# Kernel optimization log

Measured on AMD Instinct MI355X. Metric: run time of the kernel, lower is better.

Reference implementation:

```python
import jax, jax.numpy as jnp
import numpy as np

D = 128          # embedding_size
K = 1024         # num_embedding
DECAY = 0.99
EPS = 1e-5
VQ_COMMIT = 0.25
B, T = 16, 4096


def setup_inputs() -> dict:
    key = jax.random.key(0)
    k1, k2, k3 = jax.random.split(key, 3)
    emb = jax.random.normal(k2, (D, K), dtype=jnp.float32)
    return {
        "input": jax.random.normal(k1, (B, T, D), dtype=jnp.float32),
        "embedding": emb,
        "cluster_size": jnp.zeros((K,), dtype=jnp.float32),
        "embedding_mean": emb.copy(),
    }


def reference(input, embedding, cluster_size, embedding_mean):
    # ---- quantize: squared-distance argmin over codebook ----
    flatten = input.reshape(-1, D)                                   # [N, D]
    dist = ((flatten ** 2).sum(1, keepdims=True)
            - 2.0 * flatten @ embedding
            + (embedding ** 2).sum(0, keepdims=True))                # [N, K]
    embedding_ind = jnp.argmin(dist, axis=1)                         # [N]
    code = embedding_ind.reshape(input.shape[:-1])                   # [B, T]

    # ---- dequantize: codebook gather ----
    quantize = jnp.take(embedding.T, code, axis=0)                   # [B, T, D]

    # ---- EMA codebook update (training mode) ----
    N = flatten.shape[0]
    counts = jax.ops.segment_sum(jnp.ones((N,), input.dtype), embedding_ind,
                                 num_segments=K)                     # [K]
    emb_sum = jax.ops.segment_sum(flatten, embedding_ind,
                                  num_segments=K).T                  # [D, K]
    new_cluster_size = cluster_size * DECAY + (1.0 - DECAY) * counts
    new_embedding_mean = embedding_mean * DECAY + (1.0 - DECAY) * emb_sum
    n = new_cluster_size.sum()
    cs = (new_cluster_size + EPS) / (n + K * EPS) * n
    new_embedding = new_embedding_mean / cs[None, :]                 # [D, K]

    # ---- straight-through estimator + commitment loss ----
    quantize_st = input + jax.lax.stop_gradient(quantize - input)
    diff = VQ_COMMIT * jnp.mean(
        (jax.lax.stop_gradient(quantize_st) - input) ** 2)

    return (quantize_st, diff, code,
            new_embedding, new_cluster_size, new_embedding_mean)
```

## Files before the change

kernel.cpp:

```cpp
#include <hip/hip_runtime.h>
#include <hip/hip_fp16.h>
#include <math.h>

#define D_ 128
#define K_ 1024
#define N_ 65536
#define DECAY_ 0.99f
#define OMD_ 0.01f
#define EPS_ 1e-5f
#define VQC_ 0.25f
#define M1_ 0.14f
#define M2_ 0.14f
#define BIAS_ 96.0f
#define CLMIN_ 0.5f
#define CLMAX_ 508.0f
#define WSEG 32

typedef __attribute__((ext_vector_type(8))) _Float16 half8;
typedef __attribute__((ext_vector_type(4))) float f32x4;

#define WOFF_CODE  0
#define WOFF_E2    65536
#define WOFF_CNT   66560
#define WOFF_SSQ   67584
#define WOFF_RCNT  67585
#define WOFF_BASE  67648
#define WOFF_CURS  68736
#define WOFF_ORDER 69760
#define WOFF_ET    136320
#define WOFF_PART  267392
#define WOFF_CSORT 398464
#define WOFF_RLIST 791680
#define WOFF_EF    857216

#define OOFF_Q     0
#define OOFF_DIFF  8388608
#define OOFF_CODE  8388609
#define OOFF_NEMB  8454145
#define OOFF_NCS   8585217
#define OOFF_NMEAN 8586241

__device__ __forceinline__ unsigned umin32(unsigned a, unsigned b) { return a < b ? a : b; }
__device__ __forceinline__ unsigned umax32(unsigned a, unsigned b) { return a > b ? a : b; }

__device__ __forceinline__ void gld16(const unsigned short* g, unsigned short* l) {
    __builtin_amdgcn_global_load_lds(
        (const __attribute__((address_space(1))) unsigned int*)g,
        (__attribute__((address_space(3))) unsigned int*)l, 16, 0, 0);
}

__launch_bounds__(256)
__global__ void k_prep(const float* __restrict__ E, float* __restrict__ Et,
                       unsigned short* __restrict__ Ef, float* __restrict__ e2,
                       int* __restrict__ cnt, float* __restrict__ part1) {
    __shared__ float tile[128 * 17];
    __shared__ float e2s[16];
    int tid = threadIdx.x;
    int b = blockIdx.x;
    int c0 = b * 16;
    if (b == 0) {
        for (int i = tid; i < 1026; i += 256) cnt[i] = 0;
    }
    #pragma unroll
    for (int i = 0; i < 8; ++i) part1[b * 2048 + i * 256 + tid] = 0.f;
    if (tid < 16) e2s[tid] = 0.f;
    #pragma unroll
    for (int i = 0; i < 8; ++i) {
        int idx = i * 256 + tid;
        int d = idx >> 4, cc = idx & 15;
        tile[d * 17 + cc] = E[d * K_ + c0 + cc];
    }
    __syncthreads();
    #pragma unroll
    for (int i = 0; i < 8; ++i) {
        int idx = i * 256 + tid;
        int cc = idx >> 7, d = idx & 127;
        Et[(size_t)(c0 + cc) * D_ + d] = tile[d * 17 + cc];
    }
    int L = tid & 63, s = tid >> 6;
    int cc = L & 15;
    int d0 = s * 32 + ((L >> 4) << 3);
    unsigned short h[8];
    float sq = 0.f;
    #pragma unroll
    for (int j = 0; j < 8; ++j) {
        float e = tile[(d0 + j) * 17 + cc];
        sq = fmaf(e, e, sq);
        h[j] = __half_as_ushort(__float2half(-2.f * e));
    }
    int T = b * 256 + tid;
    #pragma unroll
    for (int j = 0; j < 8; ++j) Ef[T * 8 + j] = h[j];
    atomicAdd(&e2s[cc], sq);
    __syncthreads();
    if (tid < 16) {
        e2[c0 + tid] = e2s[tid];
    }
}

__launch_bounds__(512, 2)
__global__ void k_argmin_mfma(const float* __restrict__ x, const unsigned short* __restrict__ Ef,
                              const float* __restrict__ e2,
                              int* __restrict__ code_i, float* __restrict__ code_f,
                              int* __restrict__ cnt, int* __restrict__ rcnt,
                              int* __restrict__ rlist, const float* __restrict__ Et) {
    __shared__ unsigned short Bs[3][8192];
    __shared__ float e2s[K_];
    int tid = threadIdx.x;
    int w = tid >> 6, L = tid & 63, quad = L >> 4, col = L & 15;
    int mg = w >> 1, ng = w & 1;
    int n0 = blockIdx.x * 128;

    for (int i = tid; i < K_; i += 512) e2s[i] = e2[i];

    half8 ah[2][4];
    #pragma unroll
    for (int mt = 0; mt < 2; ++mt) {
        int tok = n0 + (2 * mg + mt) * 16 + col;
        #pragma unroll
        for (int s = 0; s < 4; ++s) {
            const float* p = x + (size_t)tok * D_ + s * 32 + quad * 8;
            float4 u0 = *(const float4*)(p);
            float4 u1 = *(const float4*)(p + 4);
            ah[mt][s][0] = (_Float16)u0.x; ah[mt][s][1] = (_Float16)u0.y;
            ah[mt][s][2] = (_Float16)u0.z; ah[mt][s][3] = (_Float16)u0.w;
            ah[mt][s][4] = (_Float16)u1.x; ah[mt][s][5] = (_Float16)u1.y;
            ah[mt][s][6] = (_Float16)u1.z; ah[mt][s][7] = (_Float16)u1.w;
        }
    }

    unsigned k1[2][4], k2[2][4], k3[2][4];
    #pragma unroll
    for (int mt = 0; mt < 2; ++mt)
        #pragma unroll
        for (int r = 0; r < 4; ++r) {
            k1[mt][r] = 0xFFFFFFFFu; k2[mt][r] = 0xFFFFFFFFu; k3[mt][r] = 0xFFFFFFFFu;
        }

    __syncthreads();

    #pragma unroll
    for (int i = 0; i < 2; ++i) {
        int o = (w * 2 + i) * 512;
        gld16(Ef + o + L * 8, &Bs[0][o]);
    }
    #pragma unroll
    for (int i = 0; i < 2; ++i) {
        int o = (w * 2 + i) * 512;
        gld16(Ef + 8192 + o + L * 8, &Bs[1][o]);
    }

    #pragma unroll
    for (int q = 0; q < 16; ++q) {
        if (q < 15) asm volatile("s_waitcnt vmcnt(2)" ::: "memory");
        else        asm volatile("s_waitcnt vmcnt(0)" ::: "memory");
        __builtin_amdgcn_s_barrier();
        asm volatile("" ::: "memory");

        const unsigned short* Bp = &Bs[q % 3][0];

        float evb[2];
        #pragma unroll
        for (int nn = 0; nn < 2; ++nn)
            evb[nn] = e2s[q * 64 + (2 * ng + nn) * 16 + col] + BIAS_;
        f32x4 acc[2][2];
        #pragma unroll
        for (int mt = 0; mt < 2; ++mt)
            #pragma unroll
            for (int nn = 0; nn < 2; ++nn)
                #pragma unroll
                for (int r = 0; r < 4; ++r)
                    acc[mt][nn][r] = evb[nn];

        #pragma unroll
        for (int s = 0; s < 4; ++s) {
            half8 bh[2];
            #pragma unroll
            for (int nn = 0; nn < 2; ++nn) {
                int off = (((2 * ng + nn) * 4 + s) * 64 + L) * 8;
                bh[nn] = *(const half8*)(Bp + off);
            }
            #pragma unroll
            for (int nn = 0; nn < 2; ++nn)
                #pragma unroll
                for (int mt = 0; mt < 2; ++mt)
                    acc[mt][nn] = __builtin_amdgcn_mfma_f32_16x16x32_f16(ah[mt][s], bh[nn], acc[mt][nn], 0, 0, 0);
        }

        #pragma unroll
        for (int nn = 0; nn < 2; ++nn) {
            unsigned cb = (unsigned)(q * 64 + (2 * ng + nn) * 16 + col);
            #pragma unroll
            for (int mt = 0; mt < 2; ++mt)
                #pragma unroll
                for (int r = 0; r < 4; ++r) {
                    float dc = fminf(fmaxf(acc[mt][nn][r], CLMIN_), CLMAX_);
                    unsigned key = (__float_as_uint(dc) & 0xFFFFFC00u) | cb;
                    unsigned m1 = umax32(k1[mt][r], key);
                    k1[mt][r]   = umin32(k1[mt][r], key);
                    unsigned m2 = umax32(k2[mt][r], m1);
                    k2[mt][r]   = umin32(k2[mt][r], m1);
                    k3[mt][r]   = umin32(k3[mt][r], m2);
                }
        }

        if (q < 14) {
            const unsigned short* src = Ef + (q + 2) * 8192;
            int sl = (q + 2) % 3;
            #pragma unroll
            for (int i = 0; i < 2; ++i) {
                int o = (w * 2 + i) * 512;
                gld16(src + o + L * 8, &Bs[sl][o]);
            }
        }
    }

    __syncthreads();
    unsigned* mk1 = (unsigned*)&Bs[0][0];
    unsigned* mk2 = mk1 + 256;
    unsigned* mk3 = mk2 + 256;

    #pragma unroll
    for (int mt = 0; mt < 2; ++mt) {
        #pragma unroll
        for (int r = 0; r < 4; ++r) {
            unsigned a = k1[mt][r], b = k2[mt][r], c = k3[mt][r];
            #pragma unroll
            for (int m = 1; m < 16; m <<= 1) {
                unsigned ao = (unsigned)__shfl_xor((int)a, m);
                unsigned bo = (unsigned)__shfl_xor((int)b, m);
                unsigned co = (unsigned)__shfl_xor((int)c, m);
                unsigned t1 = umax32(a, ao);
                a           = umin32(a, ao);
                unsigned s2 = umin32(b, bo);
                unsigned u  = umax32(t1, s2);
                b           = umin32(t1, s2);
                c           = umin32(u, umin32(c, co));
            }
            if (col == 0) {
                int tl = (2 * mg + mt) * 16 + quad * 4 + r;
                mk1[tl * 2 + ng] = a;
                mk2[tl * 2 + ng] = b;
                mk3[tl * 2 + ng] = c;
            }
        }
    }
    __syncthreads();
    if (tid < 128) {
        unsigned a1 = mk1[tid * 2], b1 = mk1[tid * 2 + 1];
        unsigned a2 = mk2[tid * 2], b2 = mk2[tid * 2 + 1];
        unsigned a3 = mk3[tid * 2], b3 = mk3[tid * 2 + 1];
        unsigned t1 = umax32(a1, b1);
        unsigned kk1 = umin32(a1, b1);
        unsigned s2 = umin32(a2, b2);
        unsigned kk2 = umin32(t1, s2);
        unsigned u  = umax32(t1, s2);
        unsigned kk3 = umin32(u, umin32(a3, b3));

        int i1 = (int)(kk1 & 1023u), i2 = (int)(kk2 & 1023u);
        float d1 = __uint_as_float(kk1 & 0xFFFFFC00u);
        float d2 = __uint_as_float(kk2 & 0xFFFFFC00u);
        float d3 = __uint_as_float(kk3 & 0xFFFFFC00u);
        int tok = n0 + tid;

        if (d3 - d1 < M2_) {
            code_i[tok] = i1;
            code_f[tok] = (float)i1;
            atomicAdd(cnt + i1, 1);
            int p = atomicAdd(rcnt, 1);
            rlist[p] = tok;
        } else {
            int win = i1;
            if (d2 - d1 < M1_) {
                const float* xr = x  + (size_t)tok * D_;
                const float* ea = Et + (size_t)i1 * D_;
                const float* eb = Et + (size_t)i2 * D_;
                float s1 = 0.f, sB = 0.f;
                #pragma unroll 4
                for (int dd = 0; dd < D_; dd += 4) {
                    float4 xv = *(const float4*)(xr + dd);
                    float4 av = *(const float4*)(ea + dd);
                    float4 bv = *(const float4*)(eb + dd);
                    s1 = fmaf(xv.x, av.x, s1); s1 = fmaf(xv.y, av.y, s1);
                    s1 = fmaf(xv.z, av.z, s1); s1 = fmaf(xv.w, av.w, s1);
                    sB = fmaf(xv.x, bv.x, sB); sB = fmaf(xv.y, bv.y, sB);
                    sB = fmaf(xv.z, bv.z, sB); sB = fmaf(xv.w, bv.w, sB);
                }
                float ex1 = e2s[i1] - 2.f * s1;
                float ex2 = e2s[i2] - 2.f * sB;
                if (ex2 < ex1 || (ex2 == ex1 && i2 < i1)) win = i2;
            }
            code_i[tok] = win;
            code_f[tok] = (float)win;
            atomicAdd(cnt + win, 1);
        }
    }
}

__launch_bounds__(256)
__global__ void k_fix(const float* __restrict__ x, const float* __restrict__ Et,
                      const float* __restrict__ e2, const int* __restrict__ rcnt,
                      const int* __restrict__ rlist, int* __restrict__ code_i,
                      float* __restrict__ code_f, int* __restrict__ cnt) {
    __shared__ float4 xs[32];
    __shared__ float sd[8];
    __shared__ int   si[8];
    int tid = threadIdx.x;
    int lane = tid & 63, w = tid >> 6;
    int half = lane >> 5;
    int q32  = lane & 31;
    int slot = w * 2 + half;
    int nr = *rcnt;
    for (int it = blockIdx.x; it < nr; it += gridDim.x) {
        __syncthreads();
        int tok = rlist[it];
        if (tid < 32) xs[tid] = ((const float4*)(x + (size_t)tok * D_))[tid];
        __syncthreads();
        float4 xv = xs[q32];
        float bd = INFINITY; int bb = 0;
        for (int c0 = 0; c0 < K_; c0 += 8) {
            int c = c0 + slot;
            float4 e = ((const float4*)(Et + (size_t)c * D_))[q32];
            float dot = xv.x * e.x + xv.y * e.y + xv.z * e.z + xv.w * e.w;
            dot += __shfl_xor(dot, 1);
            dot += __shfl_xor(dot, 2);
            dot += __shfl_xor(dot, 4);
            dot += __shfl_xor(dot, 8);
            dot += __shfl_xor(dot, 16);
            float dist = e2[c] - 2.f * dot;
            if (dist < bd) { bd = dist; bb = c; }
        }
        if (q32 == 0) { sd[slot] = bd; si[slot] = bb; }
        __syncthreads();
        if (tid == 0) {
            float fb = sd[0]; int fi = si[0];
            #pragma unroll
            for (int s = 1; s < 8; ++s) {
                if (sd[s] < fb || (sd[s] == fb && si[s] < fi)) { fb = sd[s]; fi = si[s]; }
            }
            int ob = code_i[tok];
            if (fi != ob) {
                code_i[tok] = fi;
                code_f[tok] = (float)fi;
                atomicAdd(cnt + ob, -1);
                atomicAdd(cnt + fi, 1);
            }
        }
    }
}

__launch_bounds__(256)
__global__ void k_scan(const int* __restrict__ cnt, int* __restrict__ base,
                       int* __restrict__ cursor) {
    int t = threadIdx.x;
    int lane = t & 63, wv = t >> 6;
    int c[4];
    #pragma unroll
    for (int j = 0; j < 4; ++j) c[j] = cnt[4 * t + j];
    int s = c[0] + c[1] + c[2] + c[3];
    int ps = s;
    #pragma unroll
    for (int m = 1; m < 64; m <<= 1) {
        int o = __shfl_up(ps, m);
        if (lane >= m) ps += o;
    }
    __shared__ int wtot[4];
    if (lane == 63) wtot[wv] = ps;
    __syncthreads();
    int woff = 0;
    for (int i = 0; i < 4; ++i) if (i < wv) woff += wtot[i];
    int run = woff + ps - s;
    #pragma unroll
    for (int j = 0; j < 4; ++j) {
        cursor[4 * t + j] = run;
        run += c[j];
        base[4 * t + j + 1] = run;
    }
    if (t == 0) base[0] = 0;
}

__global__ void k_scatter(const int* __restrict__ code_i, int* __restrict__ cursor,
                          int* __restrict__ order, int* __restrict__ csort) {
    int n = blockIdx.x * 256 + threadIdx.x;
    int c = code_i[n];
    int pos = atomicAdd(cursor + c, 1);
    order[pos] = n;
    csort[pos] = c;
}

__launch_bounds__(128)
__global__ void k_segdeq(const float* __restrict__ x, const float* __restrict__ Et,
                         const int* __restrict__ order, const int* __restrict__ csort,
                         float* __restrict__ part1, float* __restrict__ outq,
                         float* __restrict__ ssqp) {
    __shared__ int sn[WSEG], sc[WSEG];
    int d = threadIdx.x;
    int i0 = blockIdx.x * WSEG;
    if (d < WSEG) { sn[d] = order[i0 + d]; sc[d] = csort[i0 + d]; }
    __syncthreads();
    int cprev = sc[0];
    float eq = Et[(size_t)cprev * D_ + d];
    float acc = 0.f, ssql = 0.f;
    float xv = x[(size_t)sn[0] * D_ + d];
    #pragma unroll 4
    for (int j = 0; j < WSEG; ++j) {
        float xn = (j < WSEG - 1) ? x[(size_t)sn[j + 1] * D_ + d] : 0.f;
        int c = sc[j];
        if (c != cprev) {
            atomicAdd(&part1[(size_t)cprev * D_ + d], acc);
            acc = 0.f;
            eq = Et[(size_t)c * D_ + d];
            cprev = c;
        }
        float qv = xv + (eq - xv);
        outq[(size_t)sn[j] * D_ + d] = qv;
        float t = qv - xv;
        ssql = fmaf(t, t, ssql);
        acc += xv;
        xv = xn;
    }
    atomicAdd(&part1[(size_t)cprev * D_ + d], acc);

    #pragma unroll
    for (int off = 32; off > 0; off >>= 1) ssql += __shfl_down(ssql, off);
    __shared__ float wsum[2];
    if ((d & 63) == 0) wsum[d >> 6] = ssql;
    __syncthreads();
    if (d == 0) atomicAdd(ssqp, wsum[0] + wsum[1]);
}

__launch_bounds__(256)
__global__ void k_embed(const float* __restrict__ em, const float* __restrict__ part1,
                        const int* __restrict__ cnt, const float* __restrict__ csz,
                        const float* __restrict__ ssqp, float* __restrict__ out_nmean,
                        float* __restrict__ out_nemb, float* __restrict__ out_ncs,
                        float* __restrict__ out_diff) {
    int tid = threadIdx.x;
    __shared__ float red[256];

    float ls = 0.f;
    for (int j = tid; j < K_; j += 256) ls += csz[j] * DECAY_ + OMD_ * (float)cnt[j];
    red[tid] = ls;
    __syncthreads();
    for (int off = 128; off > 0; off >>= 1) {
        if (tid < off) red[tid] += red[tid + off];
        __syncthreads();
    }
    float n = red[0];
    __syncthreads();

    if (blockIdx.x == 0) {
        for (int j = tid; j < K_; j += 256)
            out_ncs[j] = csz[j] * DECAY_ + OMD_ * (float)cnt[j];
        if (tid == 0) *out_diff = VQC_ * ssqp[0] / (float)(N_ * D_);
    }

    int i = blockIdx.x * 256 + tid;
    int k = i & (K_ - 1);
    int d = i >> 10;
    float ncs_k = csz[k] * DECAY_ + OMD_ * (float)cnt[k];
    float csk = (ncs_k + EPS_) / (n + (float)K_ * EPS_) * n;
    float es = part1[(size_t)k * D_ + d];
    float nm = em[i] * DECAY_ + OMD_ * es;
    out_nmean[i] = nm;
    out_nemb[i]  = nm / csk;
}

extern "C" void kernel_launch(void* const* d_in, const int* in_sizes, int n_in,
                              void* d_out, int out_size, void* d_ws, size_t ws_size,
                              hipStream_t stream) {
    const float* x   = (const float*)d_in[0];
    const float* E   = (const float*)d_in[1];
    const float* csz = (const float*)d_in[2];
    const float* em  = (const float*)d_in[3];
    float* out = (float*)d_out;
    float* W   = (float*)d_ws;

    int*   code_i = (int*)(W + WOFF_CODE);
    float* e2     = W + WOFF_E2;
    int*   cnt    = (int*)(W + WOFF_CNT);
    float* ssqp   = W + WOFF_SSQ;
    int*   rcnt   = (int*)(W + WOFF_RCNT);
    int*   base   = (int*)(W + WOFF_BASE);
    int*   cursor = (int*)(W + WOFF_CURS);
    int*   order  = (int*)(W + WOFF_ORDER);
    float* Et     = W + WOFF_ET;
    float* part1  = W + WOFF_PART;
    int*   csort  = (int*)(W + WOFF_CSORT);
    int*   rlist  = (int*)(W + WOFF_RLIST);
    unsigned short* Ef = (unsigned short*)(W + WOFF_EF);

    k_prep<<<64, 256, 0, stream>>>(E, Et, Ef, e2, cnt, part1);
    k_argmin_mfma<<<N_ / 128, 512, 0, stream>>>(x, Ef, e2, code_i,
                                                out + OOFF_CODE, cnt, rcnt, rlist, Et);
    k_fix<<<1024, 256, 0, stream>>>(x, Et, e2, rcnt, rlist, code_i, out + OOFF_CODE, cnt);
    k_scan<<<1, 256, 0, stream>>>(cnt, base, cursor);
    k_scatter<<<N_ / 256, 256, 0, stream>>>(code_i, cursor, order, csort);
    k_segdeq<<<N_ / WSEG, 128, 0, stream>>>(x, Et, order, csort, part1,
                                            out + OOFF_Q, ssqp);
    k_embed<<<(D_ * K_) / 256, 256, 0, stream>>>(em, part1, cnt, csz, ssqp,
                                                 out + OOFF_NMEAN, out + OOFF_NEMB,
                                                 out + OOFF_NCS, out + OOFF_DIFF);
}
```

Baseline: 238.8 us.

## Pipeline argmin in paired chunks, fuse scan into scatter, widen segdeq blocks

The argmin kernel now uses a 4-slot LDS ring and issues prefetch two chunks at a time, with one barrier per pair of chunks instead of per chunk. Its launch bound is raised to 4 blocks per CU. The separate single-block scan kernel is removed: every scatter block recomputes the prefix sum into shared memory and atomically bumps a zeroed per-code counter. The segment dequant kernel uses 256 threads, with each half handling 16 tokens. These changes aim to cut barriers and a launch, at the cost of redundant scans, more LDS and register pressure, and a full vmcnt(0) wait per pair.

```diff
diff --git a/kernel.cpp b/kernel.cpp
--- a/kernel.cpp
+++ b/kernel.cpp
@@ -52,7 +52,8 @@
 __launch_bounds__(256)
 __global__ void k_prep(const float* __restrict__ E, float* __restrict__ Et,
                        unsigned short* __restrict__ Ef, float* __restrict__ e2,
-                       int* __restrict__ cnt, float* __restrict__ part1) {
+                       int* __restrict__ cnt, int* __restrict__ zc,
+                       float* __restrict__ part1) {
     __shared__ float tile[128 * 17];
     __shared__ float e2s[16];
     int tid = threadIdx.x;
@@ -61,6 +62,9 @@
     if (b == 0) {
         for (int i = tid; i < 1026; i += 256) cnt[i] = 0;
     }
+    if (b == 1) {
+        for (int i = tid; i < 1024; i += 256) zc[i] = 0;
+    }
     #pragma unroll
     for (int i = 0; i < 8; ++i) part1[b * 2048 + i * 256 + tid] = 0.f;
     if (tid < 16) e2s[tid] = 0.f;
@@ -98,13 +102,13 @@
     }
 }
 
-__launch_bounds__(512, 2)
+__launch_bounds__(512, 4)
 __global__ void k_argmin_mfma(const float* __restrict__ x, const unsigned short* __restrict__ Ef,
                               const float* __restrict__ e2,
                               int* __restrict__ code_i, float* __restrict__ code_f,
                               int* __restrict__ cnt, int* __restrict__ rcnt,
                               int* __restrict__ rlist, const float* __restrict__ Et) {
-    __shared__ unsigned short Bs[3][8192];
+    __shared__ unsigned short Bs[4][8192];
     __shared__ float e2s[K_];
     int tid = threadIdx.x;
     int w = tid >> 6, L = tid & 63, quad = L >> 4, col = L & 15;
@@ -140,77 +144,81 @@
     __syncthreads();
 
     #pragma unroll
-    for (int i = 0; i < 2; ++i) {
-        int o = (w * 2 + i) * 512;
-        gld16(Ef + o + L * 8, &Bs[0][o]);
-    }
-    #pragma unroll
-    for (int i = 0; i < 2; ++i) {
-        int o = (w * 2 + i) * 512;
-        gld16(Ef + 8192 + o + L * 8, &Bs[1][o]);
-    }
-
-    #pragma unroll
-    for (int q = 0; q < 16; ++q) {
-        if (q < 15) asm volatile("s_waitcnt vmcnt(2)" ::: "memory");
-        else        asm volatile("s_waitcnt vmcnt(0)" ::: "memory");
+    for (int c = 0; c < 2; ++c)
+        #pragma unroll
+        for (int i = 0; i < 2; ++i) {
+            int o = (w * 2 + i) * 512;
+            gld16(Ef + c * 8192 + o + L * 8, &Bs[c][o]);
+        }
+
+    #pragma unroll
+    for (int p = 0; p < 8; ++p) {
+        asm volatile("s_waitcnt vmcnt(0)" ::: "memory");
         __builtin_amdgcn_s_barrier();
         asm volatile("" ::: "memory");
 
-        const unsigned short* Bp = &Bs[q % 3][0];
-
-        float evb[2];
+        if (p < 7) {
+            #pragma unroll
+            for (int c = 0; c < 2; ++c) {
+                int ch = 2 * p + 2 + c;
+                const unsigned short* src = Ef + ch * 8192;
+                int sl = ch & 3;
+                #pragma unroll
+                for (int i = 0; i < 2; ++i) {
+                    int o = (w * 2 + i) * 512;
+                    gld16(src + o + L * 8, &Bs[sl][o]);
+                }
+            }
+        }
+
         #pragma unroll
-        for (int nn = 0; nn < 2; ++nn)
-            evb[nn] = e2s[q * 64 + (2 * ng + nn) * 16 + col] + BIAS_;
-        f32x4 acc[2][2];
-        #pragma unroll
-        for (int mt = 0; mt < 2; ++mt)
+        for (int hh = 0; hh < 2; ++hh) {
+            int q = 2 * p + hh;
+            const unsigned short* Bp = &Bs[q & 3][0];
+
+            float evb[2];
             #pragma unroll
             for (int nn = 0; nn < 2; ++nn)
+                evb[nn] = e2s[q * 64 + (2 * ng + nn) * 16 + col] + BIAS_;
+            f32x4 acc[2][2];
+            #pragma unroll
+            for (int mt = 0; mt < 2; ++mt)
                 #pragma unroll
-                for (int r = 0; r < 4; ++r)
-                    acc[mt][nn][r] = evb[nn];
-
-        #pragma unroll
-        for (int s = 0; s < 4; ++s) {
-            half8 bh[2];
+                for (int nn = 0; nn < 2; ++nn)
+                    #pragma unroll
+                    for (int r = 0; r < 4; ++r)
+                        acc[mt][nn][r] = evb[nn];
+
+            #pragma unroll
+            for (int s = 0; s < 4; ++s) {
+                half8 bh[2];
+                #pragma unroll
+                for (int nn = 0; nn < 2; ++nn) {
+                    int off = (((2 * ng + nn) * 4 + s) * 64 + L) * 8;
+                    bh[nn] = *(const half8*)(Bp + off);
+                }
+                #pragma unroll
+                for (int nn = 0; nn < 2; ++nn)
+                    #pragma unroll
+                    for (int mt = 0; mt < 2; ++mt)
+                        acc[mt][nn] = __builtin_amdgcn_mfma_f32_16x16x32_f16(ah[mt][s], bh[nn], acc[mt][nn], 0, 0, 0);
+            }
+
             #pragma unroll
             for (int nn = 0; nn < 2; ++nn) {
-                int off = (((2 * ng + nn) * 4 + s) * 64 + L) * 8;
-                bh[nn] = *(const half8*)(Bp + off);
-            }
-            #pragma unroll
-            for (int nn = 0; nn < 2; ++nn)
+                unsigned cb = (unsigned)(q * 64 + (2 * ng + nn) * 16 + col);
                 #pragma unroll
                 for (int mt = 0; mt < 2; ++mt)
-                    acc[mt][nn] = __builtin_amdgcn_mfma_f32_16x16x32_f16(ah[mt][s], bh[nn], acc[mt][nn], 0, 0, 0);
-        }
-
-        #pragma unroll
-        for (int nn = 0; nn < 2; ++nn) {
-            unsigned cb = (unsigned)(q * 64 + (2 * ng + nn) * 16 + col);
-            #pragma unroll
-            for (int mt = 0; mt < 2; ++mt)
-                #pragma unroll
-                for (int r = 0; r < 4; ++r) {
-                    float dc = fminf(fmaxf(acc[mt][nn][r], CLMIN_), CLMAX_);
-                    unsigned key = (__float_as_uint(dc) & 0xFFFFFC00u) | cb;
-                    unsigned m1 = umax32(k1[mt][r], key);
-                    k1[mt][r]   = umin32(k1[mt][r], key);
-                    unsigned m2 = umax32(k2[mt][r], m1);
-                    k2[mt][r]   = umin32(k2[mt][r], m1);
-                    k3[mt][r]   = umin32(k3[mt][r], m2);
-                }
-        }
-
-        if (q < 14) {
-            const unsigned short* src = Ef + (q + 2) * 8192;
-            int sl = (q + 2) % 3;
-            #pragma unroll
-            for (int i = 0; i < 2; ++i) {
-                int o = (w * 2 + i) * 512;
-                gld16(src + o + L * 8, &Bs[sl][o]);
+                    #pragma unroll
+                    for (int r = 0; r < 4; ++r) {
+                        float dc = fminf(fmaxf(acc[mt][nn][r], CLMIN_), CLMAX_);
+                        unsigned key = (__float_as_uint(dc) & 0xFFFFFC00u) | cb;
+                        unsigned m1 = umax32(k1[mt][r], key);
+                        k1[mt][r]   = umin32(k1[mt][r], key);
+                        unsigned m2 = umax32(k2[mt][r], m1);
+                        k2[mt][r]   = umin32(k2[mt][r], m1);
+                        k3[mt][r]   = umin32(k3[mt][r], m2);
+                    }
             }
         }
     }
@@ -350,21 +358,23 @@
 }
 
 __launch_bounds__(256)
-__global__ void k_scan(const int* __restrict__ cnt, int* __restrict__ base,
-                       int* __restrict__ cursor) {
+__global__ void k_scatter(const int* __restrict__ cnt, const int* __restrict__ code_i,
+                          int* __restrict__ zc, int* __restrict__ order,
+                          int* __restrict__ csort) {
+    __shared__ int sbase[1024];
+    __shared__ int wtot[4];
     int t = threadIdx.x;
     int lane = t & 63, wv = t >> 6;
-    int c[4];
-    #pragma unroll
-    for (int j = 0; j < 4; ++j) c[j] = cnt[4 * t + j];
-    int s = c[0] + c[1] + c[2] + c[3];
+    int c4[4];
+    #pragma unroll
+    for (int j = 0; j < 4; ++j) c4[j] = cnt[4 * t + j];
+    int s = c4[0] + c4[1] + c4[2] + c4[3];
     int ps = s;
     #pragma unroll
     for (int m = 1; m < 64; m <<= 1) {
         int o = __shfl_up(ps, m);
         if (lane >= m) ps += o;
     }
-    __shared__ int wtot[4];
     if (lane == 63) wtot[wv] = ps;
     __syncthreads();
     int woff = 0;
@@ -372,40 +382,41 @@
     int run = woff + ps - s;
     #pragma unroll
     for (int j = 0; j < 4; ++j) {
-        cursor[4 * t + j] = run;
-        run += c[j];
-        base[4 * t + j + 1] = run;
-    }
-    if (t == 0) base[0] = 0;
-}
-
-__global__ void k_scatter(const int* __restrict__ code_i, int* __restrict__ cursor,
-                          int* __restrict__ order, int* __restrict__ csort) {
-    int n = blockIdx.x * 256 + threadIdx.x;
+        sbase[4 * t + j] = run;
+        run += c4[j];
+    }
+    __syncthreads();
+
+    int n = blockIdx.x * 256 + t;
     int c = code_i[n];
-    int pos = atomicAdd(cursor + c, 1);
+    int pos = sbase[c] + atomicAdd(zc + c, 1);
     order[pos] = n;
     csort[pos] = c;
 }
 
-__launch_bounds__(128)
+__launch_bounds__(256)
 __global__ void k_segdeq(const float* __restrict__ x, const float* __restrict__ Et,
                          const int* __restrict__ order, const int* __restrict__ csort,
                          float* __restrict__ part1, float* __restrict__ outq,
                          float* __restrict__ ssqp) {
     __shared__ int sn[WSEG], sc[WSEG];
-    int d = threadIdx.x;
+    __shared__ float wsum[4];
+    int tid = threadIdx.x;
+    int d = tid & 127;
+    int h = tid >> 7;
     int i0 = blockIdx.x * WSEG;
-    if (d < WSEG) { sn[d] = order[i0 + d]; sc[d] = csort[i0 + d]; }
-    __syncthreads();
-    int cprev = sc[0];
+    if (tid < WSEG) { sn[tid] = order[i0 + tid]; sc[tid] = csort[i0 + tid]; }
+    __syncthreads();
+    int s0 = h * 16;
+    int cprev = sc[s0];
     float eq = Et[(size_t)cprev * D_ + d];
     float acc = 0.f, ssql = 0.f;
-    float xv = x[(size_t)sn[0] * D_ + d];
+    float xv = x[(size_t)sn[s0] * D_ + d];
     #pragma unroll 4
-    for (int j = 0; j < WSEG; ++j) {
-        float xn = (j < WSEG - 1) ? x[(size_t)sn[j + 1] * D_ + d] : 0.f;
-        int c = sc[j];
+    for (int j = 0; j < 16; ++j) {
+        int sj = s0 + j;
+        float xn = (j < 15) ? x[(size_t)sn[sj + 1] * D_ + d] : 0.f;
+        int c = sc[sj];
         if (c != cprev) {
             atomicAdd(&part1[(size_t)cprev * D_ + d], acc);
             acc = 0.f;
@@ -413,7 +424,7 @@
             cprev = c;
         }
         float qv = xv + (eq - xv);
-        outq[(size_t)sn[j] * D_ + d] = qv;
+        outq[(size_t)sn[sj] * D_ + d] = qv;
         float t = qv - xv;
         ssql = fmaf(t, t, ssql);
         acc += xv;
@@ -423,10 +434,9 @@
 
     #pragma unroll
     for (int off = 32; off > 0; off >>= 1) ssql += __shfl_down(ssql, off);
-    __shared__ float wsum[2];
-    if ((d & 63) == 0) wsum[d >> 6] = ssql;
-    __syncthreads();
-    if (d == 0) atomicAdd(ssqp, wsum[0] + wsum[1]);
+    if ((tid & 63) == 0) wsum[tid >> 6] = ssql;
+    __syncthreads();
+    if (tid == 0) atomicAdd(ssqp, (wsum[0] + wsum[1]) + (wsum[2] + wsum[3]));
 }
 
 __launch_bounds__(256)
@@ -481,8 +491,7 @@
     int*   cnt    = (int*)(W + WOFF_CNT);
     float* ssqp   = W + WOFF_SSQ;
     int*   rcnt   = (int*)(W + WOFF_RCNT);
-    int*   base   = (int*)(W + WOFF_BASE);
-    int*   cursor = (int*)(W + WOFF_CURS);
+    int*   zc     = (int*)(W + WOFF_CURS);
     int*   order  = (int*)(W + WOFF_ORDER);
     float* Et     = W + WOFF_ET;
     float* part1  = W + WOFF_PART;
@@ -490,13 +499,12 @@
     int*   rlist  = (int*)(W + WOFF_RLIST);
     unsigned short* Ef = (unsigned short*)(W + WOFF_EF);
 
-    k_prep<<<64, 256, 0, stream>>>(E, Et, Ef, e2, cnt, part1);
+    k_prep<<<64, 256, 0, stream>>>(E, Et, Ef, e2, cnt, zc, part1);
     k_argmin_mfma<<<N_ / 128, 512, 0, stream>>>(x, Ef, e2, code_i,
                                                 out + OOFF_CODE, cnt, rcnt, rlist, Et);
     k_fix<<<1024, 256, 0, stream>>>(x, Et, e2, rcnt, rlist, code_i, out + OOFF_CODE, cnt);
-    k_scan<<<1, 256, 0, stream>>>(cnt, base, cursor);
-    k_scatter<<<N_ / 256, 256, 0, stream>>>(code_i, cursor, order, csort);
-    k_segdeq<<<N_ / WSEG, 128, 0, stream>>>(x, Et, order, csort, part1,
+    k_scatter<<<N_ / 256, 256, 0, stream>>>(cnt, code_i, zc, order, csort);
+    k_segdeq<<<N_ / WSEG, 256, 0, stream>>>(x, Et, order, csort, part1,
                                             out + OOFF_Q, ssqp);
     k_embed<<<(D_ * K_) / 256, 256, 0, stream>>>(em, part1, cnt, csz, ssqp,
                                                  out + OOFF_NMEAN, out + OOFF_NEMB,
```

New measurement: 233.9 us. 1.02x faster.
